# Performance work log

Hardware: AMD Instinct MI355X
Metric: run time of the kernel (lower is better)

## Reference

```python
import jax, jax.numpy as jnp
import numpy as np

V = 1024      # visible_size (channel_size)
H = 2048      # hidden_size
F = V + H     # full_size
T = 64        # timesteps
REC = 0.8     # params['lambda']


def setup_inputs() -> dict:
    key = jax.random.key(0)
    k1, k2, k3 = jax.random.split(key, 3)
    X = jax.random.normal(k1, (T, V), jnp.float32)
    # scale W so tanh does not fully saturate (fan-in scaling, like default init)
    W = jax.random.normal(k2, (F, F), jnp.float32) / np.float32(np.sqrt(F))
    b = jax.random.normal(k3, (F,), jnp.float32) * 0.01
    # Lambda: visible block = REC, hidden block = 1, diagonal of visible block = 1
    lam = jnp.concatenate(
        [jnp.full((V, V), REC, jnp.float32), jnp.ones((V, H), jnp.float32)], axis=1
    )
    lam = lam.at[jnp.arange(V), jnp.arange(V)].set(1.0)
    return {"X": X, "W": W, "b": b, "lam": lam}


def reference(X, W, b, lam):
    v = lam.shape[0]           # visible size
    one_minus_lam_vis = 1.0 - lam[:, :v]  # zero outside visible block anyway

    def step(carry, x_t):
        R, _ = carry
        WR = R @ W.T + b                      # [V, F] Linear applied row-wise
        U = lam * WR                          # gated recurrent part
        # I has x_t broadcast across rows in the visible block, zeros elsewhere
        U = U.at[:, :v].add(one_minus_lam_vis * x_t[None, :])
        R_next = jnp.tanh(U)                  # phi = torch.tanh
        return (R_next, U), None

    R0 = jnp.zeros((v, W.shape[0]), X.dtype)
    (_, U_last), _ = jax.lax.scan(step, (R0, R0), X)
    # torch.diag(U[:, :visible]) -> diagonal entries, shape [V]
    idx = jnp.arange(v)
    return U_last[idx, idx]
```

## Files before the change

### kernel.cpp

```cpp
#include <hip/hip_runtime.h>
#include <math.h>

#define V 1024
#define H 2048
#define F 3072
#define T 64
#define REC 0.8f

#define BM 128
#define BN 128
#define KT16 (F / 16)
#define NSS  (KT16 / 4)

typedef _Float16 half8 __attribute__((ext_vector_type(8)));
typedef float floatx16 __attribute__((ext_vector_type(16)));

__device__ __forceinline__ void gld16(const void* g, void* l) {
    __builtin_amdgcn_global_load_lds(
        (const __attribute__((address_space(1))) void*)g,
        (__attribute__((address_space(3))) void*)l, 16, 0, 0);
}

__device__ __forceinline__ float fast_tanh(float u) {
    float e = __expf(2.f * u);
    return 1.f - 2.f * __builtin_amdgcn_rcpf(e + 1.f);
}


__global__ __launch_bounds__(256)
void conv_w_fm(const float* __restrict__ W, _Float16* __restrict__ Wfm) {
    const int ct = blockIdx.y;
    const int ix = blockIdx.x * 256 + threadIdx.x;
    const int kt = ix >> 8;
    const int q  = ix & 255;
    const int n  = ct * 128 + ((q >> 6) & 3) * 32 + (q & 31);
    const int k0 = kt * 16 + ((q >> 5) & 1) * 8;
    const float* src = W + (size_t)n * F + k0;
    float4 v0 = *(const float4*)src;
    float4 v1 = *(const float4*)(src + 4);
    half8 o = { (_Float16)v0.x, (_Float16)v0.y, (_Float16)v0.z, (_Float16)v0.w,
                (_Float16)v1.x, (_Float16)v1.y, (_Float16)v1.z, (_Float16)v1.w };
    *(half8*)(Wfm + ((size_t)(ct * KT16 + kt) * 2048 + q * 8)) = o;
}

__global__ __launch_bounds__(256)
void init_step0(const float* __restrict__ b, const float* __restrict__ x0,
                _Float16* __restrict__ Rfm) {
    const int rt = blockIdx.y;
    const int ix = blockIdx.x * 256 + threadIdx.x;
    const int kt = ix >> 8;
    const int q  = ix & 255;
    const int gi = rt * 128 + ((q >> 6) & 3) * 32 + (q & 31);
    const int k0 = kt * 16 + ((q >> 5) & 1) * 8;
    half8 o;
    #pragma unroll
    for (int e = 0; e < 8; ++e) {
        int gj = k0 + e;
        float wr = b[gj];
        float u = (gj >= V || gi == gj) ? wr : (REC * wr + (1.f - REC) * x0[gj]);
        o[e] = (_Float16)fast_tanh(u);
    }
    *(half8*)(Rfm + ((size_t)(rt * KT16 + kt) * 2048 + q * 8)) = o;
}

__global__ __launch_bounds__(512, 2)
void frnn_step(const _Float16* __restrict__ Rin, const _Float16* __restrict__ Wfm,
               const float* __restrict__ b, const float* __restrict__ xt,
               _Float16* __restrict__ Rout, float* __restrict__ out, int is_last)
{
    __shared__ _Float16 A0[8192], B0[8192];
    __shared__ _Float16 A1[8192], B1[8192];
    __shared__ _Float16 A2[8192], B2[8192];

    const int tid  = threadIdx.x;
    const int lane = tid & 63;
    const int wid  = tid >> 6;
    const int sp   = wid & 1;
    const int kg   = wid >> 1;
    const int row0 = blockIdx.y * BM;
    const int col0 = blockIdx.x * BN;
    const int lane8 = lane * 8;

    const int sq  = tid & 255;
    const int sq8 = sq * 8;
    const _Float16* sgbase = (tid < 256)
        ? Rin + ((size_t)blockIdx.y * KT16 * 2048 + sq8)
        : Wfm + ((size_t)blockIdx.x * KT16 * 2048 + sq8);

    floatx16 acc[2][4];
    #pragma unroll
    for (int i = 0; i < 2; ++i)
        #pragma unroll
        for (int j = 0; j < 4; ++j)
            #pragma unroll
            for (int r = 0; r < 16; ++r) acc[i][j][r] = 0.f;

    {
        _Float16* d0 = (tid < 256) ? &A0[sq8] : &B0[sq8];
        _Float16* d1 = (tid < 256) ? &A1[sq8] : &B1[sq8];
        #pragma unroll
        for (int g = 0; g < 4; ++g)
            gld16(sgbase + (size_t)g * 2048, d0 + g * 2048);
        asm volatile("" ::: "memory");
        #pragma unroll
        for (int g = 0; g < 4; ++g)
            gld16(sgbase + (size_t)(4 + g) * 2048, d1 + g * 2048);
    }

#define BODY(M, CA, CB, NA, NB)                                                 \
  {                                                                             \
    asm volatile("s_waitcnt vmcnt(4) lgkmcnt(0)\n\ts_barrier" ::: "memory");    \
    const _Float16* sA = &CA[kg * 2048];                                        \
    const _Float16* sB = &CB[kg * 2048];                                        \
    half8 a0 = *(const half8*)(sA + sp * 1024 + lane8);                         \
    half8 a1 = *(const half8*)(sA + sp * 1024 + 512 + lane8);                   \
    half8 b0 = *(const half8*)(sB + lane8);                                     \
    half8 b1 = *(const half8*)(sB + 512 + lane8);                               \
    half8 b2 = *(const half8*)(sB + 1024 + lane8);                              \
    half8 b3 = *(const half8*)(sB + 1536 + lane8);                              \
    asm volatile("" ::: "memory");           \
    int nxt = (M) + 2; if (nxt >= NSS) nxt -= NSS;     \
    _Float16* dst = (tid < 256) ? &NA[sq8] : &NB[sq8];                          \
    _Pragma("unroll")                                                           \
    for (int g = 0; g < 4; ++g)                                                 \
        gld16(sgbase + (size_t)(nxt * 4 + g) * 2048, dst + g * 2048);           \
    acc[0][0] = __builtin_amdgcn_mfma_f32_32x32x16_f16(a0, b0, acc[0][0],0,0,0);\
    acc[0][1] = __builtin_amdgcn_mfma_f32_32x32x16_f16(a0, b1, acc[0][1],0,0,0);\
    acc[0][2] = __builtin_amdgcn_mfma_f32_32x32x16_f16(a0, b2, acc[0][2],0,0,0);\
    acc[0][3] = __builtin_amdgcn_mfma_f32_32x32x16_f16(a0, b3, acc[0][3],0,0,0);\
    acc[1][0] = __builtin_amdgcn_mfma_f32_32x32x16_f16(a1, b0, acc[1][0],0,0,0);\
    acc[1][1] = __builtin_amdgcn_mfma_f32_32x32x16_f16(a1, b1, acc[1][1],0,0,0);\
    acc[1][2] = __builtin_amdgcn_mfma_f32_32x32x16_f16(a1, b2, acc[1][2],0,0,0);\
    acc[1][3] = __builtin_amdgcn_mfma_f32_32x32x16_f16(a1, b3, acc[1][3],0,0,0);\
  }

    #pragma unroll 1
    for (int m3 = 0; m3 < NSS / 3; ++m3) {
        const int M = m3 * 3;
        BODY(M,     A0, B0, A2, B2)
        BODY(M + 1, A1, B1, A0, B0)
        BODY(M + 2, A2, B2, A1, B1)
    }
#undef BODY

    asm volatile("s_waitcnt vmcnt(0) lgkmcnt(0)\n\ts_barrier" ::: "memory");

    const int m32 = lane & 31, hh = lane >> 5;
    float b_r[4], x_r[4];
    if (kg == 0) {
        #pragma unroll
        for (int j = 0; j < 4; ++j) {
            int gj = col0 + j * 32 + m32;
            b_r[j] = b[gj];
            x_r[j] = (gj < V) ? xt[gj] : 0.f;
        }
    }

    float* red0 = (float*)(sp ? A1 : A0);
    float* red1 = (float*)(sp ? B1 : B0);
    #pragma unroll 1
    for (int w = 1; w < 4; ++w) {
        if (kg == w) {
            #pragma unroll
            for (int j = 0; j < 4; ++j)
                #pragma unroll
                for (int q4 = 0; q4 < 4; ++q4) {
                    float4 v0 = { acc[0][j][4*q4],   acc[0][j][4*q4+1],
                                  acc[0][j][4*q4+2], acc[0][j][4*q4+3] };
                    float4 v1 = { acc[1][j][4*q4],   acc[1][j][4*q4+1],
                                  acc[1][j][4*q4+2], acc[1][j][4*q4+3] };
                    *(float4*)(red0 + (j*4 + q4) * 256 + lane * 4) = v0;
                    *(float4*)(red1 + (j*4 + q4) * 256 + lane * 4) = v1;
                }
        }
        __syncthreads();
        if (kg == 0) {
            #pragma unroll
            for (int j = 0; j < 4; ++j)
                #pragma unroll
                for (int q4 = 0; q4 < 4; ++q4) {
                    float4 v0 = *(const float4*)(red0 + (j*4 + q4) * 256 + lane * 4);
                    float4 v1 = *(const float4*)(red1 + (j*4 + q4) * 256 + lane * 4);
                    acc[0][j][4*q4]   += v0.x; acc[0][j][4*q4+1] += v0.y;
                    acc[0][j][4*q4+2] += v0.z; acc[0][j][4*q4+3] += v0.w;
                    acc[1][j][4*q4]   += v1.x; acc[1][j][4*q4+1] += v1.y;
                    acc[1][j][4*q4+2] += v1.z; acc[1][j][4*q4+3] += v1.w;
                }
        }
        __syncthreads();
    }

    if (kg == 0) {
        #pragma unroll
        for (int i = 0; i < 2; ++i) {
            const int mb = sp * 2 + i;
            #pragma unroll
            for (int j = 0; j < 4; ++j) {
                const int gj = col0 + j * 32 + m32;
                const int kt = gj >> 4;
                const int h2 = (gj >> 3) & 1;
                const int e  = gj & 7;
                _Float16* tb = Rout + ((size_t)(blockIdx.y * KT16 + kt) * 2048
                                       + (mb * 2 + h2) * 256 + e);
                const float bj = b_r[j];
                const float xj = x_r[j];
                const bool vis = (gj < V);
                #pragma unroll
                for (int r = 0; r < 16; ++r) {
                    const int mrow = 4 * hh + (r & 3) + 8 * (r >> 2);
                    const int gi = row0 + mb * 32 + mrow;
                    float wr = acc[i][j][r] + bj;
                    float u = (!vis || gi == gj) ? wr : (REC * wr + (1.f - REC) * xj);
                    tb[mrow * 8] = (_Float16)fast_tanh(u);
                    if (is_last && gi == gj) out[gi] = u;
                }
            }
        }
    }
}

extern "C" void kernel_launch(void* const* d_in, const int* in_sizes, int n_in,
                              void* d_out, int out_size, void* d_ws, size_t ws_size,
                              hipStream_t stream) {
    const float* X = (const float*)d_in[0];
    const float* W = (const float*)d_in[1];
    const float* b = (const float*)d_in[2];
    float* out = (float*)d_out;

    _Float16* Wfm = (_Float16*)d_ws;
    _Float16* Ra  = Wfm + (size_t)F * F;
    _Float16* Rb  = Ra + (size_t)V * F;

    conv_w_fm<<<dim3(192, 24), 256, 0, stream>>>(W, Wfm);
    init_step0<<<dim3(192, 8), 256, 0, stream>>>(b, X, Ra);

    for (int t = 1; t < T; ++t) {
        _Float16* Rin  = (t & 1) ? Ra : Rb;
        _Float16* Rout = (t & 1) ? Rb : Ra;
        frnn_step<<<dim3(24, 8), 512, 0, stream>>>(Rin, Wfm, b, X + (size_t)t * V,
                                                   Rout, out, t == T - 1);
    }
}
```

Baseline: 1.990 ms.

## Switch to double-buffered 128-wide K slabs with all threads loading both operands

Replaces the triple-buffered 64-wide K pipeline with a double-buffered scheme where each stage covers 128 K elements (twice the MFMAs per barrier). Every thread now issues loads for both A and B instead of splitting the block by operand. A second barrier after the LDS reads lets the next slab overwrite the buffer just consumed. This halves the number of barrier iterations, but the extra barrier per stage and the shallower prefetch depth may expose more load latency.

```diff
diff --git a/kernel.cpp b/kernel.cpp
--- a/kernel.cpp
+++ b/kernel.cpp
@@ -10,7 +10,8 @@
 #define BM 128
 #define BN 128
 #define KT16 (F / 16)
-#define NSS  (KT16 / 4)
+#define NB   (F / 128)
+#define SLABH 16384
 
 typedef _Float16 half8 __attribute__((ext_vector_type(8)));
 typedef float floatx16 __attribute__((ext_vector_type(16)));
@@ -68,9 +69,8 @@
                const float* __restrict__ b, const float* __restrict__ xt,
                _Float16* __restrict__ Rout, float* __restrict__ out, int is_last)
 {
-    __shared__ _Float16 A0[8192], B0[8192];
-    __shared__ _Float16 A1[8192], B1[8192];
-    __shared__ _Float16 A2[8192], B2[8192];
+    __shared__ _Float16 A0[SLABH], B0[SLABH];
+    __shared__ _Float16 A1[SLABH], B1[SLABH];
 
     const int tid  = threadIdx.x;
     const int lane = tid & 63;
@@ -81,11 +81,9 @@
     const int col0 = blockIdx.x * BN;
     const int lane8 = lane * 8;
 
-    const int sq  = tid & 255;
-    const int sq8 = sq * 8;
-    const _Float16* sgbase = (tid < 256)
-        ? Rin + ((size_t)blockIdx.y * KT16 * 2048 + sq8)
-        : Wfm + ((size_t)blockIdx.x * KT16 * 2048 + sq8);
+    const _Float16* gAbase = Rin + ((size_t)blockIdx.y * KT16 * 2048 + tid * 8);
+    const _Float16* gBbase = Wfm + ((size_t)blockIdx.x * KT16 * 2048 + tid * 8);
+    const int l8 = tid * 8;
 
     floatx16 acc[2][4];
     #pragma unroll
@@ -95,51 +93,66 @@
             #pragma unroll
             for (int r = 0; r < 16; ++r) acc[i][j][r] = 0.f;
 
-    {
-        _Float16* d0 = (tid < 256) ? &A0[sq8] : &B0[sq8];
-        _Float16* d1 = (tid < 256) ? &A1[sq8] : &B1[sq8];
-        #pragma unroll
-        for (int g = 0; g < 4; ++g)
-            gld16(sgbase + (size_t)g * 2048, d0 + g * 2048);
-        asm volatile("" ::: "memory");
-        #pragma unroll
-        for (int g = 0; g < 4; ++g)
-            gld16(sgbase + (size_t)(4 + g) * 2048, d1 + g * 2048);
-    }
-
-#define BODY(M, CA, CB, NA, NB)                                                 \
+    #pragma unroll
+    for (int g = 0; g < 4; ++g) {
+        gld16(gAbase + (size_t)g * 4096, &A0[l8 + g * 4096]);
+        gld16(gBbase + (size_t)g * 4096, &B0[l8 + g * 4096]);
+    }
+    asm volatile("" ::: "memory");
+    #pragma unroll
+    for (int g = 0; g < 4; ++g) {
+        gld16(gAbase + (size_t)(SLABH + g * 4096), &A1[l8 + g * 4096]);
+        gld16(gBbase + (size_t)(SLABH + g * 4096), &B1[l8 + g * 4096]);
+    }
+
+#define BODY(M, CA, CB)                                                         \
   {                                                                             \
-    asm volatile("s_waitcnt vmcnt(4) lgkmcnt(0)\n\ts_barrier" ::: "memory");    \
-    const _Float16* sA = &CA[kg * 2048];                                        \
-    const _Float16* sB = &CB[kg * 2048];                                        \
-    half8 a0 = *(const half8*)(sA + sp * 1024 + lane8);                         \
-    half8 a1 = *(const half8*)(sA + sp * 1024 + 512 + lane8);                   \
-    half8 b0 = *(const half8*)(sB + lane8);                                     \
-    half8 b1 = *(const half8*)(sB + 512 + lane8);                               \
-    half8 b2 = *(const half8*)(sB + 1024 + lane8);                              \
-    half8 b3 = *(const half8*)(sB + 1536 + lane8);                              \
-    asm volatile("" ::: "memory");           \
-    int nxt = (M) + 2; if (nxt >= NSS) nxt -= NSS;     \
-    _Float16* dst = (tid < 256) ? &NA[sq8] : &NB[sq8];                          \
+    asm volatile("s_waitcnt vmcnt(8) lgkmcnt(0)\n\ts_barrier" ::: "memory");    \
+    const _Float16* sA0 = &CA[(2 * kg)     * 2048];                             \
+    const _Float16* sA1 = &CA[(2 * kg + 1) * 2048];                             \
+    const _Float16* sB0 = &CB[(2 * kg)     * 2048];                             \
+    const _Float16* sB1 = &CB[(2 * kg + 1) * 2048];                             \
+    half8 a00 = *(const half8*)(sA0 + sp * 1024 + lane8);                       \
+    half8 a01 = *(const half8*)(sA0 + sp * 1024 + 512 + lane8);                 \
+    half8 b00 = *(const half8*)(sB0 + lane8);                                   \
+    half8 b01 = *(const half8*)(sB0 + 512 + lane8);                             \
+    half8 b02 = *(const half8*)(sB0 + 1024 + lane8);                            \
+    half8 b03 = *(const half8*)(sB0 + 1536 + lane8);                            \
+    half8 a10 = *(const half8*)(sA1 + sp * 1024 + lane8);                       \
+    half8 a11 = *(const half8*)(sA1 + sp * 1024 + 512 + lane8);                 \
+    half8 b10 = *(const half8*)(sB1 + lane8);                                   \
+    half8 b11 = *(const half8*)(sB1 + 512 + lane8);                             \
+    half8 b12 = *(const half8*)(sB1 + 1024 + lane8);                            \
+    half8 b13 = *(const half8*)(sB1 + 1536 + lane8);                            \
+    asm volatile("s_waitcnt lgkmcnt(0)\n\ts_barrier" ::: "memory");             \
+    int nxt = (M) + 2; if (nxt >= NB) nxt -= NB;       \
     _Pragma("unroll")                                                           \
-    for (int g = 0; g < 4; ++g)                                                 \
-        gld16(sgbase + (size_t)(nxt * 4 + g) * 2048, dst + g * 2048);           \
-    acc[0][0] = __builtin_amdgcn_mfma_f32_32x32x16_f16(a0, b0, acc[0][0],0,0,0);\
-    acc[0][1] = __builtin_amdgcn_mfma_f32_32x32x16_f16(a0, b1, acc[0][1],0,0,0);\
-    acc[0][2] = __builtin_amdgcn_mfma_f32_32x32x16_f16(a0, b2, acc[0][2],0,0,0);\
-    acc[0][3] = __builtin_amdgcn_mfma_f32_32x32x16_f16(a0, b3, acc[0][3],0,0,0);\
-    acc[1][0] = __builtin_amdgcn_mfma_f32_32x32x16_f16(a1, b0, acc[1][0],0,0,0);\
-    acc[1][1] = __builtin_amdgcn_mfma_f32_32x32x16_f16(a1, b1, acc[1][1],0,0,0);\
-    acc[1][2] = __builtin_amdgcn_mfma_f32_32x32x16_f16(a1, b2, acc[1][2],0,0,0);\
-    acc[1][3] = __builtin_amdgcn_mfma_f32_32x32x16_f16(a1, b3, acc[1][3],0,0,0);\
+    for (int g = 0; g < 4; ++g) {                                               \
+        gld16(gAbase + ((size_t)nxt * SLABH + g * 4096), &CA[l8 + g * 4096]);   \
+        gld16(gBbase + ((size_t)nxt * SLABH + g * 4096), &CB[l8 + g * 4096]);   \
+    }                                                                           \
+    acc[0][0] = __builtin_amdgcn_mfma_f32_32x32x16_f16(a00,b00,acc[0][0],0,0,0);\
+    acc[0][1] = __builtin_amdgcn_mfma_f32_32x32x16_f16(a00,b01,acc[0][1],0,0,0);\
+    acc[0][2] = __builtin_amdgcn_mfma_f32_32x32x16_f16(a00,b02,acc[0][2],0,0,0);\
+    acc[0][3] = __builtin_amdgcn_mfma_f32_32x32x16_f16(a00,b03,acc[0][3],0,0,0);\
+    acc[1][0] = __builtin_amdgcn_mfma_f32_32x32x16_f16(a01,b00,acc[1][0],0,0,0);\
+    acc[1][1] = __builtin_amdgcn_mfma_f32_32x32x16_f16(a01,b01,acc[1][1],0,0,0);\
+    acc[1][2] = __builtin_amdgcn_mfma_f32_32x32x16_f16(a01,b02,acc[1][2],0,0,0);\
+    acc[1][3] = __builtin_amdgcn_mfma_f32_32x32x16_f16(a01,b03,acc[1][3],0,0,0);\
+    acc[0][0] = __builtin_amdgcn_mfma_f32_32x32x16_f16(a10,b10,acc[0][0],0,0,0);\
+    acc[0][1] = __builtin_amdgcn_mfma_f32_32x32x16_f16(a10,b11,acc[0][1],0,0,0);\
+    acc[0][2] = __builtin_amdgcn_mfma_f32_32x32x16_f16(a10,b12,acc[0][2],0,0,0);\
+    acc[0][3] = __builtin_amdgcn_mfma_f32_32x32x16_f16(a10,b13,acc[0][3],0,0,0);\
+    acc[1][0] = __builtin_amdgcn_mfma_f32_32x32x16_f16(a11,b10,acc[1][0],0,0,0);\
+    acc[1][1] = __builtin_amdgcn_mfma_f32_32x32x16_f16(a11,b11,acc[1][1],0,0,0);\
+    acc[1][2] = __builtin_amdgcn_mfma_f32_32x32x16_f16(a11,b12,acc[1][2],0,0,0);\
+    acc[1][3] = __builtin_amdgcn_mfma_f32_32x32x16_f16(a11,b13,acc[1][3],0,0,0);\
   }
 
     #pragma unroll 1
-    for (int m3 = 0; m3 < NSS / 3; ++m3) {
-        const int M = m3 * 3;
-        BODY(M,     A0, B0, A2, B2)
-        BODY(M + 1, A1, B1, A0, B0)
-        BODY(M + 2, A2, B2, A1, B1)
+    for (int m2 = 0; m2 < NB / 2; ++m2) {
+        BODY(2 * m2,     A0, B0)
+        BODY(2 * m2 + 1, A1, B1)
     }
 #undef BODY
 
```

After: 2.396 ms. 1.2x slower.
